# Kernel optimization log

Measured on AMD Instinct MI355X. Metric: run time of the kernel, lower is better.

Reference implementation:

```python
import jax, jax.numpy as jnp
import numpy as np

D_MODEL = 512
N_HEADS = 8
D_FF = 2048
EPS = 1e-5


def _layernorm(x, g, b):
    mu = jnp.mean(x, axis=-1, keepdims=True)
    var = jnp.mean(jnp.square(x - mu), axis=-1, keepdims=True)
    return (x - mu) * jax.lax.rsqrt(var + EPS) * g + b


def setup_inputs() -> dict:
    key = jax.random.key(0)
    ks = jax.random.split(key, 12)
    B, N, C = 2, 2048, D_MODEL
    s = lambda fi, fo: 1.0 / np.sqrt(fi)
    inp = {
        "x": jax.random.normal(ks[0], (B, N, C), jnp.float32),
        # weights stored as [in, out] (y = x @ W + b)
        "qkv_w": jax.random.normal(ks[1], (C, 3 * C), jnp.float32) * s(C, 3 * C),
        "qkv_b": jnp.zeros((3 * C,), jnp.float32),
        "out_w": jax.random.normal(ks[2], (C, C), jnp.float32) * s(C, C),
        "out_b": jnp.zeros((C,), jnp.float32),
        "ffn_w1": jax.random.normal(ks[3], (C, D_FF), jnp.float32) * s(C, D_FF),
        "ffn_b1": jnp.zeros((D_FF,), jnp.float32),
        "ffn_w2": jax.random.normal(ks[4], (D_FF, C), jnp.float32) * s(D_FF, C),
        "ffn_b2": jnp.zeros((C,), jnp.float32),
        "n1_g": jnp.ones((C,), jnp.float32),
        "n1_b": jnp.zeros((C,), jnp.float32),
        "n2_g": jnp.ones((C,), jnp.float32),
        "n2_b": jnp.zeros((C,), jnp.float32),
        "conv_w": jax.random.normal(ks[5], (C, C, 3), jnp.float32) * s(3 * C, C),  # [out, in, k]
        "conv_b": jnp.zeros((C,), jnp.float32),
        "cn_g": jnp.ones((C,), jnp.float32),
        "cn_b": jnp.zeros((C,), jnp.float32),
    }
    return inp


def _forward(x, qkv_w, qkv_b, out_w, out_b, ffn_w1, ffn_b1, ffn_w2, ffn_b2,
             n1_g, n1_b, n2_g, n2_b, conv_w, conv_b, cn_g, cn_b):
    B, N, C = x.shape
    H, dk = N_HEADS, C // N_HEADS
    scale = 1.0 / np.sqrt(dk)

    # --- ProbSparse self-attention ---
    qkv = (x @ qkv_w + qkv_b).reshape(B, N, 3, H, dk)
    q, k, v = (jnp.moveaxis(qkv, (2, 3), (0, 2))[i] for i in range(3))  # each [B,H,N,dk]
    scores = jnp.einsum("bhnd,bhmd->bhnm", q, k) * scale  # [B,H,N,N]
    M = jnp.max(scores, axis=-1) - jnp.mean(scores, axis=-1)  # [B,H,N]
    n_top = max(1, min(int(N * 0.25), N - 1))
    _, top_idx = jax.lax.top_k(M, n_top)  # [B,H,n_top]
    bidx = jnp.arange(B)[:, None, None]
    hidx = jnp.arange(H)[None, :, None]
    row_sel = jnp.zeros((B, H, N), bool).at[bidx, hidx, top_idx].set(True)
    # rows not selected are fully masked (-1e9) -> uniform softmax, as in the original
    attn = jax.nn.softmax(jnp.where(row_sel[..., None], scores, -1e9), axis=-1)
    out = jnp.einsum("bhnm,bhmd->bhnd", attn, v)
    out = out.transpose(0, 2, 1, 3).reshape(B, N, C)
    attn_out = out @ out_w + out_b

    x = _layernorm(x + attn_out, n1_g, n1_b)

    # --- FFN (exact GELU) ---
    h = jax.nn.gelu(x @ ffn_w1 + ffn_b1, approximate=False)
    ffn_out = h @ ffn_w2 + ffn_b2
    x = _layernorm(x + ffn_out, n2_g, n2_b)

    # --- distilling conv: circular conv1d(k=3,p=1) -> maxpool(k=3,s=2,p=1) -> ELU -> LN ---
    xc = x.transpose(0, 2, 1)  # [B,C,N]
    xc = jnp.concatenate([xc[..., -1:], xc, xc[..., :1]], axis=-1)  # circular pad 1
    xc = jax.lax.conv_general_dilated(
        xc, conv_w, window_strides=(1,), padding="VALID",
        dimension_numbers=("NCH", "OIH", "NCH")) + conv_b[None, :, None]
    # maxpool k=3 s=2 p=1 (pad with -inf)
    neg = jnp.finfo(xc.dtype).min
    xc = jax.lax.reduce_window(xc, neg, jax.lax.max,
                               window_dimensions=(1, 1, 3), window_strides=(1, 1, 2),
                               padding=((0, 0), (0, 0), (1, 1)))
    x = xc.transpose(0, 2, 1)  # [B, N', C]
    x = _layernorm(jax.nn.elu(x), cn_g, cn_b)
    return x


def reference(x, qkv_w, qkv_b, out_w, out_b, ffn_w1, ffn_b1, ffn_w2, ffn_b2,
              n1_g, n1_b, n2_g, n2_b, conv_w, conv_b, cn_g, cn_b):
    return _forward(x, qkv_w, qkv_b, out_w, out_b, ffn_w1, ffn_b1, ffn_w2, ffn_b2,
                    n1_g, n1_b, n2_g, n2_b, conv_w, conv_b, cn_g, cn_b)
```

## Files before the change

### kernel.cpp

```cpp
#include <hip/hip_runtime.h>
#include <math.h>

#define NB 2
#define NN 2048
#define NC 512
#define NH 8
#define DK 64
#define DFF 2048
#define NTOP 512
#define NPOOL 1024
#define KSPLIT 4

typedef unsigned short u16;
typedef __attribute__((ext_vector_type(8))) short frag8;
typedef __attribute__((ext_vector_type(8))) _Float16 h8;
typedef __attribute__((ext_vector_type(4))) float f32x4;

static __device__ __forceinline__ u16 f2b(float f) {
    union { float f; unsigned int u; } v; v.f = f;
    unsigned int r = (v.u + 0x7fffu + ((v.u >> 16) & 1u)) >> 16;
    return (u16)r;
}
static __device__ __forceinline__ float b2f(u16 v) {
    union { unsigned u; float f; } x; x.u = ((unsigned)v) << 16; return x.f;
}
static __device__ __forceinline__ u16 f2h_bits(float f) {
    union { _Float16 h; u16 u; } v; v.h = (_Float16)f; return v.u;
}
static __device__ __forceinline__ float h2f_bits(u16 u) {
    union { u16 u; _Float16 h; } v; v.u = u; return (float)v.h;
}

template<int MODE>
__global__ __launch_bounds__(256) void mfma_gemm(const u16* __restrict__ A, int lda,
    const u16* __restrict__ Bt, const float* __restrict__ bias,
    float* __restrict__ C, u16* __restrict__ Cb, int ldc, int K, int act)
{
    __shared__ u16 As[128][72];
    __shared__ u16 Bs[128][72];
    int tid = threadIdx.x;
    int m0 = blockIdx.x * 128, n0 = blockIdx.y * 128;
    int wave = tid >> 6, lane = tid & 63;
    int ln = lane & 15, quad = lane >> 4;
    int wm = (wave >> 1) * 64, wn = (wave & 1) * 64;
    f32x4 acc[4][4] = {};
    for (int k0 = 0; k0 < K; k0 += 64) {
        #pragma unroll
        for (int i = 0; i < 4; i++) {
            int t = tid + i * 256;
            int m = t >> 3, kq = t & 7;
            size_t aoff;
            if (MODE == 1) {
                int grow = m0 + m;
                int shift = (k0 >> 9) - 1;
                int arow = (grow & ~(NN - 1)) | ((grow + shift) & (NN - 1));
                aoff = (size_t)arow * NC + ((k0 & 511) + kq * 8);
            } else {
                aoff = (size_t)(m0 + m) * lda + k0 + kq * 8;
            }
            *(uint4*)&As[m][kq * 8] = *(const uint4*)&A[aoff];
            *(uint4*)&Bs[m][kq * 8] = *(const uint4*)&Bt[(size_t)(n0 + m) * K + k0 + kq * 8];
        }
        __syncthreads();
        #pragma unroll
        for (int kk = 0; kk < 2; kk++) {
            frag8 af[4], bf[4];
            #pragma unroll
            for (int i = 0; i < 4; i++) {
                af[i] = *(const frag8*)&As[wm + i * 16 + ln][kk * 32 + quad * 8];
                bf[i] = *(const frag8*)&Bs[wn + i * 16 + ln][kk * 32 + quad * 8];
            }
            #pragma unroll
            for (int i = 0; i < 4; i++)
                #pragma unroll
                for (int j = 0; j < 4; j++)
                    acc[i][j] = __builtin_amdgcn_mfma_f32_16x16x32_bf16(
                        af[i], bf[j], acc[i][j], 0, 0, 0);
        }
        __syncthreads();
    }
    #pragma unroll
    for (int i = 0; i < 4; i++) {
        #pragma unroll
        for (int j = 0; j < 4; j++) {
            int col = n0 + wn + j * 16 + ln;
            float bv = bias ? bias[col] : 0.f;
            #pragma unroll
            for (int r = 0; r < 4; r++) {
                int row = m0 + wm + i * 16 + quad * 4 + r;
                float v = acc[i][j][r] + bv;
                if (act == 1) v = 0.5f * v * (1.0f + erff(v * 0.70710678118654752f));
                if (Cb) Cb[(size_t)row * ldc + col] = f2b(v);
                else    C[(size_t)row * ldc + col] = v;
            }
        }
    }
}

__global__ __launch_bounds__(256) void mfma_qk(const u16* __restrict__ A,
    const u16* __restrict__ Bt, const float* __restrict__ bias,
    float* __restrict__ Qh, float* __restrict__ Kh,
    u16* __restrict__ Qcat, u16* __restrict__ Kcat)
{
    __shared__ u16 As[128][72];
    __shared__ u16 Bs[128][72];
    int tid = threadIdx.x;
    int m0 = blockIdx.x * 128, n0 = blockIdx.y * 128;
    int wave = tid >> 6, lane = tid & 63;
    int ln = lane & 15, quad = lane >> 4;
    int wm = (wave >> 1) * 64, wn = (wave & 1) * 64;
    f32x4 acc[4][4] = {};
    for (int k0 = 0; k0 < 1024; k0 += 64) {
        #pragma unroll
        for (int i = 0; i < 4; i++) {
            int t = tid + i * 256;
            int m = t >> 3, kq = t & 7;
            *(uint4*)&As[m][kq * 8] = *(const uint4*)&A[(size_t)(m0 + m) * 1024 + k0 + kq * 8];
            *(uint4*)&Bs[m][kq * 8] = *(const uint4*)&Bt[(size_t)(n0 + m) * 1024 + k0 + kq * 8];
        }
        __syncthreads();
        #pragma unroll
        for (int kk = 0; kk < 2; kk++) {
            h8 af[4], bf[4];
            #pragma unroll
            for (int i = 0; i < 4; i++) {
                af[i] = *(const h8*)&As[wm + i * 16 + ln][kk * 32 + quad * 8];
                bf[i] = *(const h8*)&Bs[wn + i * 16 + ln][kk * 32 + quad * 8];
            }
            #pragma unroll
            for (int i = 0; i < 4; i++)
                #pragma unroll
                for (int j = 0; j < 4; j++)
                    acc[i][j] = __builtin_amdgcn_mfma_f32_16x16x32_f16(
                        af[i], bf[j], acc[i][j], 0, 0, 0);
        }
        __syncthreads();
    }
    #pragma unroll
    for (int i = 0; i < 4; i++) {
        #pragma unroll
        for (int j = 0; j < 4; j++) {
            int col = n0 + wn + j * 16 + ln;
            float bv = bias[col];
            int which = col >> 9;
            int h = (col >> 6) & 7, d = col & 63;
            #pragma unroll
            for (int r = 0; r < 4; r++) {
                int row = m0 + wm + i * 16 + quad * 4 + r;
                int b = row >> 11, n = row & (NN - 1);
                float v = acc[i][j][r] + bv;
                size_t off32 = ((size_t)((b << 3) + h) * NN + n) * DK + d;
                size_t offc  = ((size_t)((b << 3) + h) * NN + n) * 128 + d;
                u16 hb_ = f2h_bits(v);
                u16 lb_ = f2h_bits(v - h2f_bits(hb_));
                if (which == 0) {
                    Qh[off32] = v;
                    Qcat[offc] = hb_; Qcat[offc + 64] = lb_;
                } else {
                    Kh[off32] = v;
                    Kcat[offc] = hb_; Kcat[offc + 64] = lb_;
                }
            }
        }
    }
}

__global__ __launch_bounds__(256) void mfma_v(const u16* __restrict__ A,
    const u16* __restrict__ Bt, const float* __restrict__ bias, float* __restrict__ Vh)
{
    __shared__ u16 As[128][72];
    __shared__ u16 Bs[128][72];
    int tid = threadIdx.x;
    int m0 = blockIdx.x * 128, n0 = blockIdx.y * 128;
    int wave = tid >> 6, lane = tid & 63;
    int ln = lane & 15, quad = lane >> 4;
    int wm = (wave >> 1) * 64, wn = (wave & 1) * 64;
    f32x4 acc[4][4] = {};
    for (int k0 = 0; k0 < NC; k0 += 64) {
        #pragma unroll
        for (int i = 0; i < 4; i++) {
            int t = tid + i * 256;
            int m = t >> 3, kq = t & 7;
            *(uint4*)&As[m][kq * 8] = *(const uint4*)&A[(size_t)(m0 + m) * NC + k0 + kq * 8];
            *(uint4*)&Bs[m][kq * 8] = *(const uint4*)&Bt[(size_t)(n0 + m) * NC + k0 + kq * 8];
        }
        __syncthreads();
        #pragma unroll
        for (int kk = 0; kk < 2; kk++) {
            frag8 af[4], bf[4];
            #pragma unroll
            for (int i = 0; i < 4; i++) {
                af[i] = *(const frag8*)&As[wm + i * 16 + ln][kk * 32 + quad * 8];
                bf[i] = *(const frag8*)&Bs[wn + i * 16 + ln][kk * 32 + quad * 8];
            }
            #pragma unroll
            for (int i = 0; i < 4; i++)
                #pragma unroll
                for (int j = 0; j < 4; j++)
                    acc[i][j] = __builtin_amdgcn_mfma_f32_16x16x32_bf16(
                        af[i], bf[j], acc[i][j], 0, 0, 0);
        }
        __syncthreads();
    }
    #pragma unroll
    for (int i = 0; i < 4; i++) {
        #pragma unroll
        for (int j = 0; j < 4; j++) {
            int col = n0 + wn + j * 16 + ln;
            int h = col >> 6, d = col & 63;
            float bv = bias[col];
            #pragma unroll
            for (int r = 0; r < 4; r++) {
                int row = m0 + wm + i * 16 + quad * 4 + r;
                int b = row >> 11, n = row & (NN - 1);
                Vh[((size_t)((b << 3) + h) * NN + n) * DK + d] = acc[i][j][r] + bv;
            }
        }
    }
}

__global__ __launch_bounds__(256) void castw_t(const float* __restrict__ in,
    u16* __restrict__ out, int R, int C, int ldi, int coff)
{
    __shared__ float t[32][33];
    int c0 = blockIdx.x * 32, r0 = blockIdx.y * 32;
    int lx = threadIdx.x & 31, ly = threadIdx.x >> 5;
    #pragma unroll
    for (int i = 0; i < 4; i++)
        t[ly + i * 8][lx] = in[(size_t)(r0 + ly + i * 8) * ldi + coff + c0 + lx];
    __syncthreads();
    #pragma unroll
    for (int i = 0; i < 4; i++)
        out[(size_t)(c0 + ly + i * 8) * R + r0 + lx] = f2b(t[lx][ly + i * 8]);
}

__global__ __launch_bounds__(256) void castw_hl(const float* __restrict__ in,
    u16* __restrict__ out)
{
    __shared__ float t[32][33];
    int c0 = blockIdx.x * 32, r0 = blockIdx.y * 32;
    int lx = threadIdx.x & 31, ly = threadIdx.x >> 5;
    #pragma unroll
    for (int i = 0; i < 4; i++)
        t[ly + i * 8][lx] = in[(size_t)(r0 + ly + i * 8) * 1536 + c0 + lx];
    __syncthreads();
    #pragma unroll
    for (int i = 0; i < 4; i++) {
        float v = t[lx][ly + i * 8];
        u16 hb_ = f2h_bits(v);
        u16 lb_ = f2h_bits(v - h2f_bits(hb_));
        size_t ob = (size_t)(c0 + ly + i * 8) * 1024 + r0 + lx;
        out[ob] = hb_;
        out[ob + 512] = lb_;
    }
}

__global__ void castconvw_k(const float* __restrict__ cw, u16* __restrict__ out)
{
    int i = blockIdx.x * 256 + threadIdx.x;
    if (i >= 3 * NC * NC) return;
    int t = i % 3, ci = (i / 3) & (NC - 1), co = i / (3 * NC);
    out[(size_t)co * 1536 + t * NC + ci] = f2b(cw[i]);
}

__global__ void castx_k(const float* __restrict__ in, u16* __restrict__ xb,
                        u16* __restrict__ xcat)
{
    int i = blockIdx.x * 256 + threadIdx.x;
    if (i >= (NB * NN * NC) / 4) return;
    int m = i >> 7, kq = i & 127;
    float4 v = ((const float4*)in)[i];
    ushort4 b, h, l;
    b.x = f2b(v.x); b.y = f2b(v.y); b.z = f2b(v.z); b.w = f2b(v.w);
    h.x = f2h_bits(v.x); h.y = f2h_bits(v.y);
    h.z = f2h_bits(v.z); h.w = f2h_bits(v.w);
    l.x = f2h_bits(v.x - h2f_bits(h.x));
    l.y = f2h_bits(v.y - h2f_bits(h.y));
    l.z = f2h_bits(v.z - h2f_bits(h.z));
    l.w = f2h_bits(v.w - h2f_bits(h.w));
    ((ushort4*)xb)[i] = b;
    *(ushort4*)&xcat[(size_t)m * 1024 + kq * 4] = h;
    *(ushort4*)&xcat[(size_t)m * 1024 + 512 + kq * 4] = l;
}

__global__ __launch_bounds__(256) void castkv_k(const float* __restrict__ Kh,
    const float* __restrict__ Vh, u16* __restrict__ Kb, u16* __restrict__ Vtb)
{
    int bh = blockIdx.y;
    int n0 = blockIdx.x * 64;
    __shared__ float vt[64][68];
    int tid = threadIdx.x;
    const float* kin = Kh + ((size_t)bh * NN + n0) * DK;
    u16* kout = Kb + ((size_t)bh * NN + n0) * DK;
    const float* vin = Vh + ((size_t)bh * NN + n0) * DK;
    #pragma unroll
    for (int i = 0; i < 4; i++) {
        int t = tid + i * 256;
        int n = t >> 4, dq = t & 15;
        float4 v = *(const float4*)&kin[(size_t)n * DK + dq * 4];
        ushort4 o;
        o.x = f2b(v.x); o.y = f2b(v.y); o.z = f2b(v.z); o.w = f2b(v.w);
        *(ushort4*)&kout[(size_t)n * DK + dq * 4] = o;
        float4 w = *(const float4*)&vin[(size_t)n * DK + dq * 4];
        vt[dq * 4 + 0][n] = w.x; vt[dq * 4 + 1][n] = w.y;
        vt[dq * 4 + 2][n] = w.z; vt[dq * 4 + 3][n] = w.w;
    }
    __syncthreads();
    #pragma unroll
    for (int i = 0; i < 4; i++) {
        int t = tid + i * 256;
        int d = t >> 4, nq = t & 15;
        float4 v = *(const float4*)&vt[d][nq * 4];
        ushort4 o;
        o.x = f2b(v.x); o.y = f2b(v.y); o.z = f2b(v.z); o.w = f2b(v.w);
        *(ushort4*)&Vtb[((size_t)bh * DK + d) * NN + n0 + nq * 4] = o;
    }
}

__global__ __launch_bounds__(256) void meanv_part_k(const float* __restrict__ Vh,
    float* __restrict__ pmean)
{
    int bh = blockIdx.y, chunk = blockIdx.x;
    int tid = threadIdx.x;
    int d = tid & 63, sub = tid >> 6;
    const float* vb = Vh + ((size_t)bh * NN + chunk * 64 + sub * 16) * DK;
    float s = 0.f;
    #pragma unroll
    for (int r = 0; r < 16; r++) s += vb[(size_t)r * DK + d];
    __shared__ float red[256];
    red[tid] = s;
    __syncthreads();
    if (sub == 0)
        pmean[((size_t)bh * 32 + chunk) * 64 + d] =
            red[d] + red[64 + d] + red[128 + d] + red[192 + d];
}

__global__ void meanv_comb_k(const float* __restrict__ pmean, float* __restrict__ meanv)
{
    int bh = blockIdx.x;
    int d = threadIdx.x;
    float s = 0.f;
    #pragma unroll
    for (int c = 0; c < 32; c++) s += pmean[((size_t)bh * 32 + c) * 64 + d];
    meanv[bh * DK + d] = s * (1.0f / (float)NN);
}

__global__ __launch_bounds__(256) void rowstat_mfma_k(const u16* __restrict__ Qcat,
    const u16* __restrict__ Kcat, float* __restrict__ Marr, float* __restrict__ rowmax)
{
    int bh = blockIdx.x;
    int m0 = blockIdx.y * 64;
    int tid = threadIdx.x;
    int wave = tid >> 6, lane = tid & 63;
    int ln = lane & 15, quad = lane >> 4;
    __shared__ u16 Ks[128][136];
    h8 qf[4];
    {
        const u16* qp = &Qcat[((size_t)bh * NN + m0 + wave * 16 + ln) * 128];
        #pragma unroll
        for (int ks = 0; ks < 4; ks++)
            qf[ks] = *(const h8*)&qp[ks * 32 + quad * 8];
    }
    f32x4 vmax, vsum;
    #pragma unroll
    for (int r = 0; r < 4; r++) { vmax[r] = -INFINITY; vsum[r] = 0.f; }
    const u16* kB = Kcat + (size_t)bh * NN * 128;
    for (int nc = 0; nc < NN; nc += 128) {
        __syncthreads();
        #pragma unroll
        for (int i = 0; i < 8; i++) {
            int e = tid + i * 256;
            int n = e >> 4, kq = e & 15;
            *(uint4*)&Ks[n][kq * 8] = *(const uint4*)&kB[(size_t)(nc + n) * 128 + kq * 8];
        }
        __syncthreads();
        f32x4 accS[8] = {};
        #pragma unroll
        for (int nt = 0; nt < 8; nt++) {
            #pragma unroll
            for (int ks = 0; ks < 4; ks++) {
                h8 kf = *(const h8*)&Ks[nt * 16 + ln][ks * 32 + quad * 8];
                accS[nt] = __builtin_amdgcn_mfma_f32_16x16x32_f16(
                    qf[ks], kf, accS[nt], 0, 0, 0);
            }
        }
        #pragma unroll
        for (int nt = 0; nt < 8; nt++)
            #pragma unroll
            for (int r = 0; r < 4; r++) {
                vmax[r] = fmaxf(vmax[r], accS[nt][r]);
                vsum[r] += accS[nt][r];
            }
    }
    #pragma unroll
    for (int r = 0; r < 4; r++) {
        float mx = vmax[r], sm = vsum[r];
        #pragma unroll
        for (int off = 1; off < 16; off <<= 1) {
            mx = fmaxf(mx, __shfl_xor(mx, off));
            sm += __shfl_xor(sm, off);
        }
        if (ln == 0) {
            int m = m0 + wave * 16 + quad * 4 + r;
            Marr[(size_t)bh * NN + m] = (mx - sm * (1.0f / (float)NN)) * 0.125f;
            rowmax[(size_t)bh * NN + m] = mx * 0.125f;
        }
    }
}

__global__ __launch_bounds__(256) void topk_k(const float* __restrict__ Marr,
                                              int* __restrict__ idx)
{
    int bh = blockIdx.x;
    const float* Mr = Marr + (size_t)bh * NN;
    int* idxr = idx + (size_t)bh * NTOP;
    __shared__ int hist[256];
    __shared__ int suf[256];
    __shared__ int wred[4], wred2[4];
    __shared__ int bin_sh, rank_sh;
    int tid = threadIdx.x;
    int lane = tid & 63, w = tid >> 6;
    unsigned prefix = 0;
    int rank = NTOP;
    for (int pass = 0; pass < 4; pass++) {
        int shift = 24 - pass * 8;
        unsigned mask_hi = (pass == 0) ? 0u : (0xFFFFFFFFu << (shift + 8));
        hist[tid] = 0;
        __syncthreads();
        for (int i = tid; i < NN; i += 256) {
            union { float f; unsigned u; } v; v.f = Mr[i];
            unsigned k = (v.u & 0x80000000u) ? ~v.u : (v.u | 0x80000000u);
            if ((k & mask_hi) == prefix)
                atomicAdd(&hist[(k >> shift) & 255], 1);
        }
        __syncthreads();
        int v = hist[tid];
        #pragma unroll
        for (int off = 1; off < 64; off <<= 1) {
            int t = __shfl_down(v, off);
            if (lane + off < 64) v += t;
        }
        if (lane == 0) wred[w] = v;
        __syncthreads();
        int add = 0;
        #pragma unroll
        for (int w2 = 0; w2 < 4; w2++) if (w2 > w) add += wred[w2];
        suf[tid] = v + add;
        __syncthreads();
        int sv = suf[tid];
        int nxt = (tid < 255) ? suf[tid + 1] : 0;
        if (sv >= rank && nxt < rank) { bin_sh = tid; rank_sh = rank - nxt; }
        __syncthreads();
        prefix |= ((unsigned)bin_sh << shift);
        rank = rank_sh;
        __syncthreads();
    }
    union { unsigned u; float f; } tv;
    tv.u = (prefix & 0x80000000u) ? (prefix & 0x7FFFFFFFu) : ~prefix;
    float thr = tv.f;
    int lg = 0, le = 0;
    #pragma unroll
    for (int k = 0; k < 8; k++) {
        float v = Mr[tid * 8 + k];
        lg += (v > thr) ? 1 : 0;
        le += (v == thr) ? 1 : 0;
    }
    int vg = lg, ve = le;
    #pragma unroll
    for (int off = 1; off < 64; off <<= 1) {
        int tg = __shfl_up(vg, off);
        int te = __shfl_up(ve, off);
        if (lane >= off) { vg += tg; ve += te; }
    }
    if (lane == 63) { wred[w] = vg; wred2[w] = ve; }
    __syncthreads();
    int addg = 0, adde = 0, totg = 0;
    #pragma unroll
    for (int w2 = 0; w2 < 4; w2++) {
        totg += wred[w2];
        if (w2 < w) { addg += wred[w2]; adde += wred2[w2]; }
    }
    int cnt_gt = totg;
    int needed = NTOP - cnt_gt;
    int gpre = (vg + addg) - lg, epre = (ve + adde) - le;
    #pragma unroll
    for (int k = 0; k < 8; k++) {
        int p = tid * 8 + k;
        float v = Mr[p];
        bool isgt = v > thr, iseq = v == thr;
        bool selv = isgt || (iseq && epre < needed);
        if (selv) idxr[gpre + (epre < needed ? epre : needed)] = p;
        gpre += isgt ? 1 : 0;
        epre += iseq ? 1 : 0;
    }
}

__global__ void fill_k(const float* __restrict__ meanv, u16* __restrict__ ctxb)
{
    int i = blockIdx.x * 256 + threadIdx.x;
    if (i >= NB * NN * NC) return;
    int c = i & (NC - 1);
    int m = i >> 9;
    int b = m >> 11;
    int h = c >> 6, d = c & 63;
    ctxb[i] = f2b(meanv[(((b << 3) + h) << 6) + d]);
}

__global__ __launch_bounds__(256) void attn_mfma_k(const float* __restrict__ Qh,
    const u16* __restrict__ Kb, const u16* __restrict__ Vtb,
    const int* __restrict__ idx, const float* __restrict__ rowmax,
    float* __restrict__ Opart, float* __restrict__ ml)
{
    int yy = blockIdx.x;
    int bh = yy >> 2, split = yy & (KSPLIT - 1);
    int t0 = blockIdx.y * 64;
    int tid = threadIdx.x;
    int wave = tid >> 6, lane = tid & 63;
    int ln = lane & 15, quad = lane >> 4;
    __shared__ u16 Ks[128][72];
    __shared__ u16 Vt[64][136];
    __shared__ u16 Ps[4][16][136];
    __shared__ int rows[64];
    if (tid < 64) rows[tid] = idx[bh * NTOP + t0 + tid];
    __syncthreads();
    frag8 qf[2];
    {
        const float* qp = &Qh[((size_t)bh * NN + rows[wave * 16 + ln]) * DK];
        #pragma unroll
        for (int ks = 0; ks < 2; ks++) {
            float4 a = *(const float4*)&qp[ks * 32 + quad * 8];
            float4 b = *(const float4*)&qp[ks * 32 + quad * 8 + 4];
            union { frag8 f; u16 s[8]; } u;
            u.s[0] = f2b(a.x * 0.125f); u.s[1] = f2b(a.y * 0.125f);
            u.s[2] = f2b(a.z * 0.125f); u.s[3] = f2b(a.w * 0.125f);
            u.s[4] = f2b(b.x * 0.125f); u.s[5] = f2b(b.y * 0.125f);
            u.s[6] = f2b(b.z * 0.125f); u.s[7] = f2b(b.w * 0.125f);
            qf[ks] = u.f;
        }
    }
    float rm[4];
    #pragma unroll
    for (int r = 0; r < 4; r++)
        rm[r] = rowmax[(size_t)bh * NN + rows[wave * 16 + quad * 4 + r]];
    f32x4 accO[4] = {};
    float lrun[4] = {};
    const u16* kbB = Kb + (size_t)bh * NN * DK;
    const u16* vtB = Vtb + (size_t)bh * DK * NN;
    int nc0 = split * (NN / KSPLIT);
    for (int nc = nc0; nc < nc0 + NN / KSPLIT; nc += 128) {
        __syncthreads();
        #pragma unroll
        for (int i = 0; i < 4; i++) {
            int e = tid + i * 256;
            int n = e >> 3, kq = e & 7;
            *(uint4*)&Ks[n][kq * 8] = *(const uint4*)&kbB[(size_t)(nc + n) * DK + kq * 8];
        }
        #pragma unroll
        for (int i = 0; i < 4; i++) {
            int e = tid + i * 256;
            int d = e >> 4, nq = e & 15;
            *(uint4*)&Vt[d][nq * 8] = *(const uint4*)&vtB[(size_t)d * NN + nc + nq * 8];
        }
        __syncthreads();
        f32x4 accS[8] = {};
        #pragma unroll
        for (int nt = 0; nt < 8; nt++) {
            frag8 b0 = *(const frag8*)&Ks[nt * 16 + ln][quad * 8];
            frag8 b1 = *(const frag8*)&Ks[nt * 16 + ln][32 + quad * 8];
            accS[nt] = __builtin_amdgcn_mfma_f32_16x16x32_bf16(qf[0], b0, accS[nt], 0, 0, 0);
            accS[nt] = __builtin_amdgcn_mfma_f32_16x16x32_bf16(qf[1], b1, accS[nt], 0, 0, 0);
        }
        #pragma unroll
        for (int nt = 0; nt < 8; nt++)
            #pragma unroll
            for (int r = 0; r < 4; r++) {
                float p = expf(accS[nt][r] - rm[r]);
                accS[nt][r] = p;
                lrun[r] += p;
            }
        #pragma unroll
        for (int nt = 0; nt < 8; nt++)
            #pragma unroll
            for (int r = 0; r < 4; r++)
                Ps[wave][quad * 4 + r][nt * 16 + ln] = f2b(accS[nt][r]);
        #pragma unroll
        for (int ks = 0; ks < 4; ks++) {
            frag8 pf = *(const frag8*)&Ps[wave][ln][ks * 32 + quad * 8];
            #pragma unroll
            for (int nt2 = 0; nt2 < 4; nt2++) {
                frag8 vf = *(const frag8*)&Vt[nt2 * 16 + ln][ks * 32 + quad * 8];
                accO[nt2] = __builtin_amdgcn_mfma_f32_16x16x32_bf16(pf, vf, accO[nt2], 0, 0, 0);
            }
        }
    }
    #pragma unroll
    for (int r = 0; r < 4; r++) {
        float ls = lrun[r];
        #pragma unroll
        for (int off = 1; off < 16; off <<= 1) ls += __shfl_xor(ls, off);
        int p = t0 + wave * 16 + quad * 4 + r;
        size_t pb = ((size_t)bh * NTOP + p) * KSPLIT + split;
        #pragma unroll
        for (int nt2 = 0; nt2 < 4; nt2++)
            Opart[pb * 64 + nt2 * 16 + ln] = accO[nt2][r];
        if (ln == 0) ml[pb * 2 + 1] = ls;
    }
}

__global__ __launch_bounds__(256) void attn_comb_k(const float* __restrict__ Opart,
    const float* __restrict__ ml, const int* __restrict__ idx,
    u16* __restrict__ ctxb)
{
    int gid = blockIdx.x * 4 + (threadIdx.x >> 6);
    int lane = threadIdx.x & 63;
    int bh = gid >> 9;
    int h = bh & 7, b = bh >> 3;
    size_t base = (size_t)gid * KSPLIT;
    float L = 0.f, O = 0.f;
    #pragma unroll
    for (int s = 0; s < KSPLIT; s++) {
        L += ml[(base + s) * 2 + 1];
        O += Opart[(base + s) * 64 + lane];
    }
    int n = idx[gid];
    ctxb[((size_t)(b * NN + n)) * NC + h * DK + lane] = f2b(O / L);
}

__global__ __launch_bounds__(256) void ln_k(const float* __restrict__ A,
    const float* __restrict__ Bv, const u16* __restrict__ Bvb,
    const float* __restrict__ g, const float* __restrict__ bb,
    float* __restrict__ out, u16* __restrict__ outb)
{
    int row = blockIdx.x;
    int tid = threadIdx.x;
    __shared__ float v[NC];
    __shared__ float red[256];
    size_t base = (size_t)row * NC;
    for (int i = tid; i < NC; i += 256)
        v[i] = A[base + i] + (Bvb ? b2f(Bvb[base + i]) : Bv[base + i]);
    __syncthreads();
    float ls = 0.f;
    for (int i = tid; i < NC; i += 256) ls += v[i];
    red[tid] = ls; __syncthreads();
    for (int off = 128; off > 0; off >>= 1) {
        if (tid < off) red[tid] += red[tid + off];
        __syncthreads();
    }
    float mu = red[0] / (float)NC;
    __syncthreads();
    float lv = 0.f;
    for (int i = tid; i < NC; i += 256) { float d = v[i] - mu; lv += d * d; }
    red[tid] = lv; __syncthreads();
    for (int off = 128; off > 0; off >>= 1) {
        if (tid < off) red[tid] += red[tid + off];
        __syncthreads();
    }
    float rstd = rsqrtf(red[0] / (float)NC + 1e-5f);
    for (int i = tid; i < NC; i += 256) {
        float r = (v[i] - mu) * rstd * g[i] + bb[i];
        if (out) out[base + i] = r;
        if (outb) outb[base + i] = f2b(r);
    }
}

__global__ __launch_bounds__(256) void pool_ln_k(const u16* __restrict__ y,
    const float* __restrict__ g, const float* __restrict__ bb,
    float* __restrict__ outp)
{
    int row = blockIdx.x;
    int j = row & (NPOOL - 1), b = row / NPOOL;
    int tid = threadIdx.x;
    __shared__ float v[NC];
    __shared__ float red[256];
    const u16* ybase = y + (size_t)b * NN * NC;
    for (int i = tid; i < NC; i += 256) {
        float m = -INFINITY;
        int p0 = 2 * j - 1;
        #pragma unroll
        for (int t = 0; t < 3; t++) {
            int p = p0 + t;
            if (p >= 0 && p < NN) m = fmaxf(m, b2f(ybase[(size_t)p * NC + i]));
        }
        v[i] = m > 0.f ? m : expm1f(m);
    }
    __syncthreads();
    float ls = 0.f;
    for (int i = tid; i < NC; i += 256) ls += v[i];
    red[tid] = ls; __syncthreads();
    for (int off = 128; off > 0; off >>= 1) {
        if (tid < off) red[tid] += red[tid + off];
        __syncthreads();
    }
    float mu = red[0] / (float)NC;
    __syncthreads();
    float lv = 0.f;
    for (int i = tid; i < NC; i += 256) { float d = v[i] - mu; lv += d * d; }
    red[tid] = lv; __syncthreads();
    for (int off = 128; off > 0; off >>= 1) {
        if (tid < off) red[tid] += red[tid + off];
        __syncthreads();
    }
    float rstd = rsqrtf(red[0] / (float)NC + 1e-5f);
    for (int i = tid; i < NC; i += 256)
        outp[(size_t)row * NC + i] = (v[i] - mu) * rstd * g[i] + bb[i];
}

extern "C" void kernel_launch(void* const* d_in, const int* in_sizes, int n_in,
                              void* d_out, int out_size, void* d_ws, size_t ws_size,
                              hipStream_t stream)
{
    (void)in_sizes; (void)n_in; (void)out_size; (void)ws_size;
    const float* x      = (const float*)d_in[0];
    const float* qkv_w  = (const float*)d_in[1];
    const float* qkv_b  = (const float*)d_in[2];
    const float* out_w  = (const float*)d_in[3];
    const float* out_b  = (const float*)d_in[4];
    const float* ffn_w1 = (const float*)d_in[5];
    const float* ffn_b1 = (const float*)d_in[6];
    const float* ffn_w2 = (const float*)d_in[7];
    const float* ffn_b2 = (const float*)d_in[8];
    const float* n1_g   = (const float*)d_in[9];
    const float* n1_b   = (const float*)d_in[10];
    const float* n2_g   = (const float*)d_in[11];
    const float* n2_b   = (const float*)d_in[12];
    const float* conv_w = (const float*)d_in[13];
    const float* conv_b = (const float*)d_in[14];
    const float* cn_g   = (const float*)d_in[15];
    const float* cn_b   = (const float*)d_in[16];

    const size_t R = (size_t)NB * NN * NC;
    float* ws = (float*)d_ws;
    float* x1   = ws;
    float* reg2 = ws + R;
    float* Qh   = ws + 2 * R;
    float* Kh   = ws + 3 * R;
    float* Vh   = ws + 4 * R;
    size_t o = 5 * R;
    float* pmax  = ws + o;  o += 65536;
    float* psum  = ws + o;  o += 65536;
    float* Marr  = ws + o;  o += 32768;
    float* pmean = ws + o;  o += 32768;
    float* meanv = ws + o;  o += 1024;
    int*   idx   = (int*)(ws + o);  o += 8192;
    float* ml    = ws + o;  o += 65536;
    u16*   ctxb  = (u16*)(ws + o);  o += R / 2;
    u16*   x1b   = (u16*)(ws + o);  o += R / 2;
    u16*   x2b   = (u16*)(ws + o);  o += R / 2;
    u16*   owT   = (u16*)(ws + o);  o += 131072;
    u16*   w1T   = (u16*)(ws + o);  o += 524288;
    u16*   w2T   = (u16*)(ws + o);  o += 524288;
    u16*   cwT   = (u16*)(ws + o);  o += 393216;
    u16*   xb    = (u16*)reg2;
    u16*   vwT   = (u16*)(ws + R + R / 2);
    u16*   Kb    = (u16*)reg2;
    u16*   Vtb   = (u16*)(ws + R + R / 2);
    float* Opart    = x1;
    float* attn_out = Qh;
    u16*   hb       = (u16*)(ws + 3 * R);
    u16*   ffn_outb = ctxb;
    u16*   convyb   = x1b;
    float* rowmax   = pmax;
    u16*   xcat  = (u16*)Vh;
    u16*   wcatT = w1T;
    u16*   Qcat  = x1b;
    u16*   Kcat  = (u16*)x1;
    (void)psum;

    castw_t<<<dim3(16, 16), 256, 0, stream>>>(out_w, owT, 512, 512, 512, 0);
    castw_t<<<dim3(16, 64), 256, 0, stream>>>(ffn_w2, w2T, 2048, 512, 512, 0);
    castw_t<<<dim3(16, 16), 256, 0, stream>>>(qkv_w, vwT, 512, 512, 1536, 1024);
    castconvw_k<<<3072, 256, 0, stream>>>(conv_w, cwT);
    castx_k<<<2048, 256, 0, stream>>>(x, xb, xcat);
    castw_hl<<<dim3(32, 16), 256, 0, stream>>>(qkv_w, wcatT);

    mfma_qk<<<dim3(32, 8), 256, 0, stream>>>(xcat, wcatT, qkv_b, Qh, Kh, Qcat, Kcat);

    castw_t<<<dim3(64, 16), 256, 0, stream>>>(ffn_w1, w1T, 512, 2048, 2048, 0);
    mfma_v<<<dim3(32, 4), 256, 0, stream>>>(xb, vwT, qkv_b + 1024, Vh);

    castkv_k<<<dim3(NN / 64, NB * NH), 256, 0, stream>>>(Kh, Vh, Kb, Vtb);

    meanv_part_k<<<dim3(32, NB * NH), 256, 0, stream>>>(Vh, pmean);
    meanv_comb_k<<<NB * NH, 64, 0, stream>>>(pmean, meanv);

    rowstat_mfma_k<<<dim3(NB * NH, NN / 64), 256, 0, stream>>>(Qcat, Kcat, Marr, rowmax);
    topk_k<<<NB * NH, 256, 0, stream>>>(Marr, idx);
    fill_k<<<((int)R + 255) / 256, 256, 0, stream>>>(meanv, ctxb);
    attn_mfma_k<<<dim3(NB * NH * KSPLIT, NTOP / 64), 256, 0, stream>>>(
        Qh, Kb, Vtb, idx, rowmax, Opart, ml);
    attn_comb_k<<<NB * NH * NTOP / 4, 256, 0, stream>>>(Opart, ml, idx, ctxb);

    mfma_gemm<0><<<dim3(32, 4), 256, 0, stream>>>(
        ctxb, NC, owT, out_b, attn_out, (u16*)nullptr, NC, NC, 0);

    ln_k<<<NB * NN, 256, 0, stream>>>(x, attn_out, (const u16*)nullptr,
                                      n1_g, n1_b, x1, x1b);

    mfma_gemm<0><<<dim3(32, 16), 256, 0, stream>>>(
        x1b, NC, w1T, ffn_b1, (float*)nullptr, hb, DFF, NC, 1);
    mfma_gemm<0><<<dim3(32, 4), 256, 0, stream>>>(
        hb, DFF, w2T, ffn_b2, (float*)nullptr, ffn_outb, NC, DFF, 0);

    ln_k<<<NB * NN, 256, 0, stream>>>(x1, (const float*)nullptr, ffn_outb,
                                      n2_g, n2_b, (float*)nullptr, x2b);

    mfma_gemm<1><<<dim3(32, 4), 256, 0, stream>>>(
        x2b, NC, cwT, conv_b, (float*)nullptr, convyb, NC, 1536, 0);

    pool_ln_k<<<NB * NPOOL, 256, 0, stream>>>(convyb, cn_g, cn_b, (float*)d_out);
}
```

Before: 375.4 us.

## Split-K the N=512 GEMMs into two partials and fuse reduction into LayerNorm

```diff
diff --git a/kernel.cpp b/kernel.cpp
--- a/kernel.cpp
+++ b/kernel.cpp
@@ -92,6 +92,71 @@
                 if (act == 1) v = 0.5f * v * (1.0f + erff(v * 0.70710678118654752f));
                 if (Cb) Cb[(size_t)row * ldc + col] = f2b(v);
                 else    C[(size_t)row * ldc + col] = v;
+            }
+        }
+    }
+}
+
+template<int MODE>
+__global__ __launch_bounds__(256) void mfma_gemm_sk(const u16* __restrict__ A, int lda,
+    const u16* __restrict__ Bt, float* __restrict__ P0, float* __restrict__ P1,
+    int ldc, int K)
+{
+    __shared__ u16 As[128][72];
+    __shared__ u16 Bs[128][72];
+    int tid = threadIdx.x;
+    int m0 = blockIdx.x * 128, n0 = blockIdx.y * 128;
+    int split = blockIdx.z;
+    int K2 = K >> 1, kbeg = split * K2;
+    int wave = tid >> 6, lane = tid & 63;
+    int ln = lane & 15, quad = lane >> 4;
+    int wm = (wave >> 1) * 64, wn = (wave & 1) * 64;
+    f32x4 acc[4][4] = {};
+    for (int k0 = kbeg; k0 < kbeg + K2; k0 += 64) {
+        #pragma unroll
+        for (int i = 0; i < 4; i++) {
+            int t = tid + i * 256;
+            int m = t >> 3, kq = t & 7;
+            size_t aoff;
+            if (MODE == 1) {
+                int grow = m0 + m;
+                int shift = (k0 >> 9) - 1;
+                int arow = (grow & ~(NN - 1)) | ((grow + shift) & (NN - 1));
+                aoff = (size_t)arow * NC + ((k0 & 511) + kq * 8);
+            } else {
+                aoff = (size_t)(m0 + m) * lda + k0 + kq * 8;
+            }
+            *(uint4*)&As[m][kq * 8] = *(const uint4*)&A[aoff];
+            *(uint4*)&Bs[m][kq * 8] = *(const uint4*)&Bt[(size_t)(n0 + m) * K + k0 + kq * 8];
+        }
+        __syncthreads();
+        #pragma unroll
+        for (int kk = 0; kk < 2; kk++) {
+            frag8 af[4], bf[4];
+            #pragma unroll
+            for (int i = 0; i < 4; i++) {
+                af[i] = *(const frag8*)&As[wm + i * 16 + ln][kk * 32 + quad * 8];
+                bf[i] = *(const frag8*)&Bs[wn + i * 16 + ln][kk * 32 + quad * 8];
+            }
+            #pragma unroll
+            for (int i = 0; i < 4; i++)
+                #pragma unroll
+                for (int j = 0; j < 4; j++)
+                    acc[i][j] = __builtin_amdgcn_mfma_f32_16x16x32_bf16(
+                        af[i], bf[j], acc[i][j], 0, 0, 0);
+        }
+        __syncthreads();
+    }
+    float* P = split ? P1 : P0;
+    #pragma unroll
+    for (int i = 0; i < 4; i++) {
+        #pragma unroll
+        for (int j = 0; j < 4; j++) {
+            int col = n0 + wn + j * 16 + ln;
+            #pragma unroll
+            for (int r = 0; r < 4; r++) {
+                int row = m0 + wm + i * 16 + quad * 4 + r;
+                P[(size_t)row * ldc + col] = acc[i][j][r];
             }
         }
     }
@@ -627,7 +692,8 @@
 }
 
 __global__ __launch_bounds__(256) void ln_k(const float* __restrict__ A,
-    const float* __restrict__ Bv, const u16* __restrict__ Bvb,
+    const float* __restrict__ P0, const float* __restrict__ P1,
+    const float* __restrict__ cb,
     const float* __restrict__ g, const float* __restrict__ bb,
     float* __restrict__ out, u16* __restrict__ outb)
 {
@@ -637,7 +703,7 @@
     __shared__ float red[256];
     size_t base = (size_t)row * NC;
     for (int i = tid; i < NC; i += 256)
-        v[i] = A[base + i] + (Bvb ? b2f(Bvb[base + i]) : Bv[base + i]);
+        v[i] = A[base + i] + P0[base + i] + P1[base + i] + cb[i];
     __syncthreads();
     float ls = 0.f;
     for (int i = tid; i < NC; i += 256) ls += v[i];
@@ -663,7 +729,8 @@
     }
 }
 
-__global__ __launch_bounds__(256) void pool_ln_k(const u16* __restrict__ y,
+__global__ __launch_bounds__(256) void pool_ln_k(const float* __restrict__ P0,
+    const float* __restrict__ P1, const float* __restrict__ cb,
     const float* __restrict__ g, const float* __restrict__ bb,
     float* __restrict__ outp)
 {
@@ -672,14 +739,18 @@
     int tid = threadIdx.x;
     __shared__ float v[NC];
     __shared__ float red[256];
-    const u16* ybase = y + (size_t)b * NN * NC;
+    size_t bbase = (size_t)b * NN * NC;
     for (int i = tid; i < NC; i += 256) {
         float m = -INFINITY;
         int p0 = 2 * j - 1;
+        float cbv = cb[i];
         #pragma unroll
         for (int t = 0; t < 3; t++) {
             int p = p0 + t;
-            if (p >= 0 && p < NN) m = fmaxf(m, b2f(ybase[(size_t)p * NC + i]));
+            if (p >= 0 && p < NN) {
+                size_t off = bbase + (size_t)p * NC + i;
+                m = fmaxf(m, P0[off] + P1[off] + cbv);
+            }
         }
         v[i] = m > 0.f ? m : expm1f(m);
     }
@@ -755,11 +826,10 @@
     u16*   Kb    = (u16*)reg2;
     u16*   Vtb   = (u16*)(ws + R + R / 2);
     float* Opart    = x1;
-    float* attn_out = Qh;
     u16*   hb       = (u16*)(ws + 3 * R);
-    u16*   ffn_outb = ctxb;
-    u16*   convyb   = x1b;
     float* rowmax   = pmax;
+    float* skP0 = reg2;
+    float* skP1 = Vh;
     u16*   xcat  = (u16*)Vh;
     u16*   wcatT = w1T;
     u16*   Qcat  = x1b;
@@ -790,22 +860,22 @@
         Qh, Kb, Vtb, idx, rowmax, Opart, ml);
     attn_comb_k<<<NB * NH * NTOP / 4, 256, 0, stream>>>(Opart, ml, idx, ctxb);
 
-    mfma_gemm<0><<<dim3(32, 4), 256, 0, stream>>>(
-        ctxb, NC, owT, out_b, attn_out, (u16*)nullptr, NC, NC, 0);
-
-    ln_k<<<NB * NN, 256, 0, stream>>>(x, attn_out, (const u16*)nullptr,
-                                      n1_g, n1_b, x1, x1b);
+    mfma_gemm_sk<0><<<dim3(32, 4, 2), 256, 0, stream>>>(
+        ctxb, NC, owT, skP0, skP1, NC, NC);
+
+    ln_k<<<NB * NN, 256, 0, stream>>>(x, skP0, skP1, out_b, n1_g, n1_b, x1, x1b);
 
     mfma_gemm<0><<<dim3(32, 16), 256, 0, stream>>>(
         x1b, NC, w1T, ffn_b1, (float*)nullptr, hb, DFF, NC, 1);
-    mfma_gemm<0><<<dim3(32, 4), 256, 0, stream>>>(
-        hb, DFF, w2T, ffn_b2, (float*)nullptr, ffn_outb, NC, DFF, 0);
-
-    ln_k<<<NB * NN, 256, 0, stream>>>(x1, (const float*)nullptr, ffn_outb,
+    mfma_gemm_sk<0><<<dim3(32, 4, 2), 256, 0, stream>>>(
+        hb, DFF, w2T, skP0, skP1, NC, DFF);
+
+    ln_k<<<NB * NN, 256, 0, stream>>>(x1, skP0, skP1, ffn_b2,
                                       n2_g, n2_b, (float*)nullptr, x2b);
 
-    mfma_gemm<1><<<dim3(32, 4), 256, 0, stream>>>(
-        x2b, NC, cwT, conv_b, (float*)nullptr, convyb, NC, 1536, 0);
-
-    pool_ln_k<<<NB * NPOOL, 256, 0, stream>>>(convyb, cn_g, cn_b, (float*)d_out);
-}
+    mfma_gemm_sk<1><<<dim3(32, 4, 2), 256, 0, stream>>>(
+        x2b, NC, cwT, skP0, skP1, NC, 1536);
+
+    pool_ln_k<<<NB * NPOOL, 256, 0, stream>>>(skP0, skP1, conv_b, cn_g, cn_b,
+                                              (float*)d_out);
+}
```

After: 343.5 us. 1.09x faster.
